# Optimization experiments

Measured on AMD Instinct MI355X. Metric: run time of the kernel, lower is better.

Reference implementation:

```python
import jax, jax.numpy as jnp
import numpy as np

D_MODEL = 1024
NUM_HEADS = 16
SCALE = (D_MODEL // NUM_HEADS) ** -0.5


def setup_inputs() -> dict:
    key = jax.random.key(0)
    ks = jax.random.split(key, 9)
    B, S, D = 4, 2048, D_MODEL
    s = 1.0 / np.sqrt(D)
    x = jax.random.normal(ks[0], (B, S, D), dtype=jnp.float32)
    Wq = jax.random.uniform(ks[1], (D, D), jnp.float32, -s, s)
    bq = jax.random.uniform(ks[2], (D,), jnp.float32, -s, s)
    Wk = jax.random.uniform(ks[3], (D, D), jnp.float32, -s, s)
    bk = jax.random.uniform(ks[4], (D,), jnp.float32, -s, s)
    Wv = jax.random.uniform(ks[5], (D, D), jnp.float32, -s, s)
    bv = jax.random.uniform(ks[6], (D,), jnp.float32, -s, s)
    Wo = jax.random.uniform(ks[7], (D, D), jnp.float32, -s, s)
    bo = jax.random.uniform(ks[8], (D,), jnp.float32, -s, s)
    return {"x": x, "Wq": Wq, "bq": bq, "Wk": Wk, "bk": bk,
            "Wv": Wv, "bv": bv, "Wo": Wo, "bo": bo}


def reference(x, Wq, bq, Wk, bk, Wv, bv, Wo, bo):
    # Linear: x @ W.T + b (torch nn.Linear convention)
    Q = jnp.einsum('bsd,ed->bse', x, Wq) + bq
    K = jnp.einsum('bsd,ed->bse', x, Wk) + bk
    V = jnp.einsum('bsd,ed->bse', x, Wv) + bv
    # Single-head full attention over d_model (module does NOT split heads)
    scores = jnp.einsum('bqd,bkd->bqk', Q, K) * SCALE  # [B,S,S]
    attn = jax.nn.softmax(scores, axis=-1)  # dropout is identity at inference
    out = jnp.einsum('bqk,bkd->bqd', attn, V)
    return jnp.einsum('bsd,ed->bse', out, Wo) + bo
```

## Files before the change

kernel.cpp:

```cpp
#include <hip/hip_runtime.h>
#include <hip/hip_bf16.h>


#define TILE 128
#define BK 32
#define BUFE (TILE * BK)

typedef __attribute__((ext_vector_type(8))) short bf16x8;
typedef __attribute__((ext_vector_type(4))) float f32x4;

__device__ __forceinline__ void stage_tiles(
    const __hip_bfloat16* __restrict__ Ab, const __hip_bfloat16* __restrict__ Bb,
    __hip_bfloat16* As, __hip_bfloat16* Bs,
    long rowBase, long colBase, int K, int k0, int tid)
{
  #pragma unroll
  for (int p = 0; p < 2; ++p) {
    int seg = tid + p * 256;
    int r   = seg >> 2;
    int cq  = seg & 3;
    const __hip_bfloat16* ga = Ab + (rowBase + r) * (long)K + k0 + cq * 8;
    __builtin_amdgcn_global_load_lds(
        (const __attribute__((address_space(1))) void*)ga,
        (__attribute__((address_space(3))) void*)(As + seg * 8), 16, 0, 0);
    const __hip_bfloat16* gb = Bb + (colBase + r) * (long)K + k0 + cq * 8;
    __builtin_amdgcn_global_load_lds(
        (const __attribute__((address_space(1))) void*)gb,
        (__attribute__((address_space(3))) void*)(Bs + seg * 8), 16, 0, 0);
  }
}

__device__ __forceinline__ void gemm_core(
    const __hip_bfloat16* __restrict__ Ab, const __hip_bfloat16* __restrict__ Bb,
    __hip_bfloat16* As, __hip_bfloat16* Bs,
    long rowBase, long colBase, int K, int tid, int wr, int wc, int lr, int q,
    f32x4 acc[4][4])
{
  stage_tiles(Ab, Bb, As, Bs, rowBase, colBase, K, 0, tid);
  int buf = 0;
  for (int k0 = 0; k0 < K; k0 += BK, buf ^= 1) {
    __syncthreads();
    if (k0 + BK < K)
      stage_tiles(Ab, Bb, As + (buf ^ 1) * BUFE, Bs + (buf ^ 1) * BUFE,
                  rowBase, colBase, K, k0 + BK, tid);
    const __hip_bfloat16* Ac = As + buf * BUFE;
    const __hip_bfloat16* Bc = Bs + buf * BUFE;
    bf16x8 af[4], bfr[4];
    #pragma unroll
    for (int mi = 0; mi < 4; ++mi)
      af[mi] = *(const bf16x8*)(Ac + (wr + mi * 16 + lr) * BK + q * 8);
    #pragma unroll
    for (int ni = 0; ni < 4; ++ni)
      bfr[ni] = *(const bf16x8*)(Bc + (wc + ni * 16 + lr) * BK + q * 8);
    #pragma unroll
    for (int mi = 0; mi < 4; ++mi)
      #pragma unroll
      for (int ni = 0; ni < 4; ++ni)
        acc[mi][ni] = __builtin_amdgcn_mfma_f32_16x16x32_bf16(
            af[mi], bfr[ni], acc[mi][ni], 0, 0, 0);
  }
}

__global__ __launch_bounds__(256) void gemm_bt(
    const __hip_bfloat16* __restrict__ A,
    const __hip_bfloat16* __restrict__ B,
    void* __restrict__ Cv,
    const float* __restrict__ bias,
    int K, int ldC,
    long sA, long sB, long sC,
    float scale, int mode)
{
  const long z = blockIdx.z;
  __shared__ __hip_bfloat16 As[2 * BUFE];
  __shared__ __hip_bfloat16 Bs[2 * BUFE];
  const int tid  = threadIdx.x;
  const int lane = tid & 63;
  const int wid  = tid >> 6;
  const int wr   = (wid >> 1) * 64;
  const int wc   = (wid & 1) * 64;
  const int lr   = lane & 15;
  const int q    = lane >> 4;
  const long rowBase = (long)blockIdx.x * TILE;
  const long colBase = (long)blockIdx.y * TILE;

  f32x4 acc[4][4] = {};
  gemm_core(A + z * sA, B + z * sB, As, Bs, rowBase, colBase, K,
            tid, wr, wc, lr, q, acc);

  #pragma unroll
  for (int ni = 0; ni < 4; ++ni) {
    long col = colBase + wc + ni * 16 + lr;
    float bv = bias ? bias[col] : 0.0f;
    #pragma unroll
    for (int mi = 0; mi < 4; ++mi) {
      #pragma unroll
      for (int i = 0; i < 4; ++i) {
        long row = rowBase + wr + mi * 16 + q * 4 + i;
        float v = acc[mi][ni][i] * scale + bv;
        if (mode == 0)
          ((__hip_bfloat16*)Cv)[z * sC + row * (long)ldC + col] = __float2bfloat16(v);
        else
          ((float*)Cv)[z * sC + row * (long)ldC + col] = v;
      }
    }
  }
}

__device__ __forceinline__ void stage_half(
    const __hip_bfloat16* __restrict__ g, __hip_bfloat16* lds,
    long rowBase, int ld, int k0, int tid)
{
  #pragma unroll
  for (int j = 0; j < 2; ++j) {
    int idx = tid + j * 512;
    int r   = idx >> 3;
    int cg  = (idx & 7) ^ (r & 7);
    const __hip_bfloat16* src = g + (rowBase + r) * (long)ld + k0 + cg * 8;
    __builtin_amdgcn_global_load_lds(
        (const __attribute__((address_space(1))) void*)src,
        (__attribute__((address_space(3))) void*)(lds + idx * 8), 16, 0, 0);
  }
}

__device__ __forceinline__ bf16x8 frag256(const __hip_bfloat16* half_, int row, int off)
{
  const char* p = (const char*)half_ + row * 128 + (off ^ ((row & 7) << 4));
  return *(const bf16x8*)p;
}

#define WAITV(N) asm volatile("s_waitcnt vmcnt(" #N ")" ::: "memory")
#define BAR __builtin_amdgcn_s_barrier()

__device__ __forceinline__ void xcd_decode(int NX, int NY, int NZ,
                                           int& bx, int& by, long& z)
{
  const int nwg = NX * NY * NZ;
  int lin = (int)blockIdx.x + NX * ((int)blockIdx.y + NY * (int)blockIdx.z);
  int xcd = lin & 7, off = lin >> 3;
  int q8 = nwg >> 3, r8 = nwg & 7;
  lin = ((xcd < r8) ? xcd * (q8 + 1) : r8 * (q8 + 1) + (xcd - r8) * q8) + off;
  by = lin % NY;
  bx = (lin / NY) % NX;
  z  = lin / (NY * NX);
}

#define READ_A8(BUF, HALF)                                                  \
  _Pragma("unroll")                                                         \
  for (int ks = 0; ks < 2; ++ks)                                            \
    _Pragma("unroll")                                                       \
    for (int mi = 0; mi < 4; ++mi)                                          \
      a[ks * 4 + mi] =                                                      \
          frag256(&L[BUF][0][HALF][0], wr + mi * 16 + lr, ks * 64 + q16);

#define READ_B4(BREG, BUF, HALF)                                            \
  _Pragma("unroll")                                                         \
  for (int ks = 0; ks < 2; ++ks)                                            \
    _Pragma("unroll")                                                       \
    for (int ni = 0; ni < 2; ++ni)                                          \
      BREG[ks * 2 + ni] =                                                   \
          frag256(&L[BUF][1][HALF][0], wc + ni * 16 + lr, ks * 64 + q16);

#define MMA_QUAD(MOFF, NOFF, BREG)                                          \
  __builtin_amdgcn_s_setprio(1);                                            \
  _Pragma("unroll")                                                         \
  for (int ks = 0; ks < 2; ++ks)                                            \
    _Pragma("unroll")                                                       \
    for (int mi = 0; mi < 4; ++mi)                                          \
      _Pragma("unroll")                                                     \
      for (int ni = 0; ni < 2; ++ni)                                        \
        acc[(MOFF) + mi][(NOFF) + ni] =                                     \
            __builtin_amdgcn_mfma_f32_16x16x32_bf16(                        \
                a[ks * 4 + mi], BREG[ks * 2 + ni],                          \
                acc[(MOFF) + mi][(NOFF) + ni], 0, 0, 0);                    \
  __builtin_amdgcn_s_setprio(0);

__global__ __launch_bounds__(512, 2) void gemm256_bt(
    const __hip_bfloat16* __restrict__ A,
    const __hip_bfloat16* __restrict__ B,
    void* __restrict__ Cv,
    const float* __restrict__ bias,
    int K, int ldA, int ldB, int ldC,
    long sA_, long sB_, long sC_,
    float scale, int mode)
{
  __shared__ __hip_bfloat16 L[2][2][2][128 * 64];

  const int tid  = threadIdx.x;
  const int lane = tid & 63;
  const int wid  = tid >> 6;
  const int wr   = (wid >> 2) * 64;
  const int wc   = (wid & 3) * 32;
  const int lr   = lane & 15;
  const int q    = lane >> 4;
  const int q16  = q * 16;

  int bx, by; long z;
  xcd_decode(gridDim.x, gridDim.y, gridDim.z, bx, by, z);

  const long rowBase = (long)bx * 256;
  const long colBase = (long)by * 256;
  const __hip_bfloat16* Ab = A + z * sA_;
  const __hip_bfloat16* Bb = B + z * sB_;

  f32x4 acc[8][4] = {};
  bf16x8 a[8], bA[4], bB[4];
  const int KT = K >> 6;

  {
    const int kk1 = (KT > 1 ? 1 : 0) * 64;
    stage_half(Ab, &L[0][0][0][0], rowBase,       ldA, 0,   tid);
    stage_half(Bb, &L[0][1][0][0], colBase,       ldB, 0,   tid);
    stage_half(Bb, &L[0][1][1][0], colBase + 128, ldB, 0,   tid);
    stage_half(Ab, &L[0][0][1][0], rowBase + 128, ldA, 0,   tid);
    stage_half(Ab, &L[1][0][0][0], rowBase,       ldA, kk1, tid);
    stage_half(Bb, &L[1][1][0][0], colBase,       ldB, kk1, tid);
    WAITV(8);
    BAR;
  }

  for (int kt = 0; kt < KT; ++kt) {
    const int cur = kt & 1, nxt = cur ^ 1;
    const int t1 = kt + 1 < KT ? kt + 1 : KT - 1;
    const int t2 = kt + 2 < KT ? kt + 2 : KT - 1;
    const int k1 = t1 << 6, k2 = t2 << 6;

    stage_half(Bb, &L[nxt][1][1][0], colBase + 128, ldB, k1, tid);
    WAITV(8);
    READ_A8(cur, 0);
    READ_B4(bA, cur, 0);
    BAR;
    MMA_QUAD(0, 0, bA);
    stage_half(Ab, &L[nxt][0][1][0], rowBase + 128, ldA, k1, tid);
    WAITV(8);
    READ_B4(bB, cur, 1);
    BAR;
    MMA_QUAD(0, 2, bB);
    stage_half(Ab, &L[cur][0][0][0], rowBase, ldA, k2, tid);
    WAITV(8);
    READ_A8(cur, 1);
    BAR;
    MMA_QUAD(4, 2, bB);
    stage_half(Bb, &L[cur][1][0][0], colBase, ldB, k2, tid);
    WAITV(8);
    BAR;
    MMA_QUAD(4, 0, bA);
  }
  WAITV(0);

  const long cz = z * sC_;
  #pragma unroll
  for (int n = 0; n < 4; ++n) {
    long col = colBase + (n >> 1) * 128 + wc + (n & 1) * 16 + lr;
    float bv = bias ? bias[col] : 0.0f;
    #pragma unroll
    for (int m = 0; m < 8; ++m) {
      long row0 = rowBase + (m >> 2) * 128 + wr + (m & 3) * 16 + q * 4;
      f32x4 v = acc[m][n];
      #pragma unroll
      for (int i = 0; i < 4; ++i) {
        float val = v[i] * scale + bv;
        if (mode == 0)
          ((__hip_bfloat16*)Cv)[cz + (row0 + i) * (long)ldC + col] =
              __float2bfloat16(val);
        else
          ((float*)Cv)[cz + (row0 + i) * (long)ldC + col] = val;
      }
    }
  }
}

__global__ __launch_bounds__(512, 2) void gemm128_bt(
    const __hip_bfloat16* __restrict__ A,
    const __hip_bfloat16* __restrict__ B,
    void* __restrict__ Cv,
    const float* __restrict__ bias,
    int K, int ldA, int ldB, int ldC,
    long sA_, long sB_, long sC_,
    float scale, int mode)
{
  __shared__ __hip_bfloat16 L[3][3][128 * 64];

  const int tid  = threadIdx.x;
  const int lane = tid & 63;
  const int wid  = tid >> 6;
  const int wr   = (wid >> 2) * 64;
  const int wc   = (wid & 3) * 32;
  const int lr   = lane & 15;
  const int q    = lane >> 4;
  const int q16  = q * 16;

  int bx, by; long z;
  xcd_decode(gridDim.x, gridDim.y, gridDim.z, bx, by, z);

  const long rowBase = (long)bx * 128;
  const long colBase = (long)by * 256;
  const __hip_bfloat16* Ab = A + z * sA_;
  const __hip_bfloat16* Bb = B + z * sB_;

  f32x4 acc[4][4] = {};
  bf16x8 a[8], bA[4], bB[4];
  const int KT = K >> 6;

  {
    const int kk1 = (KT > 1 ? 1 : 0) * 64;
    stage_half(Ab, &L[0][0][0], rowBase,       ldA, 0,   tid);
    stage_half(Bb, &L[0][1][0], colBase,       ldB, 0,   tid);
    stage_half(Bb, &L[0][2][0], colBase + 128, ldB, 0,   tid);
    stage_half(Ab, &L[1][0][0], rowBase,       ldA, kk1, tid);
    stage_half(Bb, &L[1][1][0], colBase,       ldB, kk1, tid);
    stage_half(Bb, &L[1][2][0], colBase + 128, ldB, kk1, tid);
    WAITV(8);
    BAR;
  }

  int cur = 0, nx2 = 2;
  for (int t = 0; t < KT; ++t) {
    const int kc = ((t + 2 < KT) ? (t + 2) : (KT - 1)) << 6;
    stage_half(Ab, &L[nx2][0][0], rowBase,       ldA, kc, tid);
    stage_half(Bb, &L[nx2][1][0], colBase,       ldB, kc, tid);
    WAITV(10);
    #pragma unroll
    for (int ks = 0; ks < 2; ++ks)
      #pragma unroll
      for (int mi = 0; mi < 4; ++mi)
        a[ks * 4 + mi] = frag256(&L[cur][0][0], wr + mi * 16 + lr, ks * 64 + q16);
    #pragma unroll
    for (int ks = 0; ks < 2; ++ks)
      #pragma unroll
      for (int ni = 0; ni < 2; ++ni)
        bA[ks * 2 + ni] = frag256(&L[cur][1][0], wc + ni * 16 + lr, ks * 64 + q16);
    BAR;
    __builtin_amdgcn_s_setprio(1);
    #pragma unroll
    for (int ks = 0; ks < 2; ++ks)
      #pragma unroll
      for (int mi = 0; mi < 4; ++mi)
        #pragma unroll
        for (int ni = 0; ni < 2; ++ni)
          acc[mi][ni] = __builtin_amdgcn_mfma_f32_16x16x32_bf16(
              a[ks * 4 + mi], bA[ks * 2 + ni], acc[mi][ni], 0, 0, 0);
    __builtin_amdgcn_s_setprio(0);
    stage_half(Bb, &L[nx2][2][0], colBase + 128, ldB, kc, tid);
    WAITV(8);
    #pragma unroll
    for (int ks = 0; ks < 2; ++ks)
      #pragma unroll
      for (int ni = 0; ni < 2; ++ni)
        bB[ks * 2 + ni] = frag256(&L[cur][2][0], wc + ni * 16 + lr, ks * 64 + q16);
    BAR;
    __builtin_amdgcn_s_setprio(1);
    #pragma unroll
    for (int ks = 0; ks < 2; ++ks)
      #pragma unroll
      for (int mi = 0; mi < 4; ++mi)
        #pragma unroll
        for (int ni = 0; ni < 2; ++ni)
          acc[mi][2 + ni] = __builtin_amdgcn_mfma_f32_16x16x32_bf16(
              a[ks * 4 + mi], bB[ks * 2 + ni], acc[mi][2 + ni], 0, 0, 0);
    __builtin_amdgcn_s_setprio(0);
    cur = (cur == 2) ? 0 : cur + 1;
    nx2 = (nx2 == 2) ? 0 : nx2 + 1;
  }
  WAITV(0);

  const long cz = z * sC_;
  #pragma unroll
  for (int n = 0; n < 4; ++n) {
    long col = colBase + (n >> 1) * 128 + wc + (n & 1) * 16 + lr;
    float bv = bias ? bias[col] : 0.0f;
    #pragma unroll
    for (int m = 0; m < 4; ++m) {
      long row0 = rowBase + wr + m * 16 + q * 4;
      f32x4 v = acc[m][n];
      #pragma unroll
      for (int i = 0; i < 4; ++i) {
        float val = v[i] * scale + bv;
        if (mode == 0)
          ((__hip_bfloat16*)Cv)[cz + (row0 + i) * (long)ldC + col] =
              __float2bfloat16(val);
        else
          ((float*)Cv)[cz + (row0 + i) * (long)ldC + col] = val;
      }
    }
  }
}

__global__ __launch_bounds__(256) void cvt_f32_bf16(
    const float* __restrict__ in, __hip_bfloat16* __restrict__ out)
{
  long i = ((long)blockIdx.x * 256 + threadIdx.x) * 8;
  float4 a = *(const float4*)(in + i);
  float4 b = *(const float4*)(in + i + 4);
  bf16x8 o;
  o[0] = __builtin_bit_cast(short, __float2bfloat16(a.x));
  o[1] = __builtin_bit_cast(short, __float2bfloat16(a.y));
  o[2] = __builtin_bit_cast(short, __float2bfloat16(a.z));
  o[3] = __builtin_bit_cast(short, __float2bfloat16(a.w));
  o[4] = __builtin_bit_cast(short, __float2bfloat16(b.x));
  o[5] = __builtin_bit_cast(short, __float2bfloat16(b.y));
  o[6] = __builtin_bit_cast(short, __float2bfloat16(b.z));
  o[7] = __builtin_bit_cast(short, __float2bfloat16(b.w));
  *(bf16x8*)(out + i) = o;
}

__global__ __launch_bounds__(256) void cvt_t_f32_bf16(
    const float* __restrict__ in, __hip_bfloat16* __restrict__ out)
{
  __shared__ __hip_bfloat16 t[64][65];
  const int tid = threadIdx.x;
  const long rb = (long)blockIdx.y * 64;
  const long cb = (long)blockIdx.x * 64;
  const int r0 = tid >> 4;
  const int c0 = (tid & 15) * 4;
  #pragma unroll
  for (int p = 0; p < 4; ++p) {
    int r = r0 + p * 16;
    float4 v = *(const float4*)(in + (rb + r) * 1024 + cb + c0);
    t[c0 + 0][r] = __float2bfloat16(v.x);
    t[c0 + 1][r] = __float2bfloat16(v.y);
    t[c0 + 2][r] = __float2bfloat16(v.z);
    t[c0 + 3][r] = __float2bfloat16(v.w);
  }
  __syncthreads();
  #pragma unroll
  for (int p = 0; p < 4; ++p) {
    int r = r0 + p * 16;
    __hip_bfloat16* o = out + (cb + r) * 1024 + rb + c0;
    o[0] = t[r][c0 + 0]; o[1] = t[r][c0 + 1];
    o[2] = t[r][c0 + 2]; o[3] = t[r][c0 + 3];
  }
}

__global__ __launch_bounds__(256) void bias_vo(
    const float* __restrict__ Wo, const float* __restrict__ bv,
    const float* __restrict__ bo, float* __restrict__ bfinal)
{
  int e = blockIdx.x * 4 + (threadIdx.x >> 6);
  int lane = threadIdx.x & 63;
  const float* row = Wo + (long)e * 1024;
  float s = 0.0f;
  #pragma unroll
  for (int p = 0; p < 4; ++p) {
    float4 w = *(const float4*)(row + p * 256 + lane * 4);
    float4 b = *(const float4*)(bv + p * 256 + lane * 4);
    s += w.x * b.x + w.y * b.y + w.z * b.z + w.w * b.w;
  }
  #pragma unroll
  for (int o = 32; o; o >>= 1) s += __shfl_xor(s, o);
  if (lane == 0) bfinal[e] = s + bo[e];
}

__global__ __launch_bounds__(256) void cat_bias(
    const float* __restrict__ a, const float* __restrict__ b,
    float* __restrict__ o)
{
  int i = blockIdx.x * 256 + threadIdx.x;
  o[i] = (i < 1024) ? a[i] : b[i - 1024];
}

__global__ __launch_bounds__(256) void softmax_rows(__hip_bfloat16* __restrict__ P)
{
  const int tid  = threadIdx.x;
  const int lane = tid & 63;
  const int wid  = tid >> 6;
  __hip_bfloat16* p = P + (long)blockIdx.x * 2048 + tid * 8;

  bf16x8 v = *(const bf16x8*)p;
  float x[8];
  #pragma unroll
  for (int i = 0; i < 8; ++i)
    x[i] = __uint_as_float(((unsigned)(unsigned short)v[i]) << 16);

  float m = x[0];
  #pragma unroll
  for (int i = 1; i < 8; ++i) m = fmaxf(m, x[i]);
  #pragma unroll
  for (int o = 32; o; o >>= 1) m = fmaxf(m, __shfl_xor(m, o));

  __shared__ float rmax[4], rsum[4];
  if (lane == 0) rmax[wid] = m;
  __syncthreads();
  m = fmaxf(fmaxf(rmax[0], rmax[1]), fmaxf(rmax[2], rmax[3]));

  float e[8], s = 0.0f;
  #pragma unroll
  for (int i = 0; i < 8; ++i) { e[i] = __expf(x[i] - m); s += e[i]; }
  #pragma unroll
  for (int o = 32; o; o >>= 1) s += __shfl_xor(s, o);
  if (lane == 0) rsum[wid] = s;
  __syncthreads();
  s = (rsum[0] + rsum[1]) + (rsum[2] + rsum[3]);

  float inv = 1.0f / s;
  bf16x8 ov;
  #pragma unroll
  for (int i = 0; i < 8; ++i) {
    __hip_bfloat16 h = __float2bfloat16(e[i] * inv);
    ov[i] = __builtin_bit_cast(short, h);
  }
  *(bf16x8*)p = ov;
}

extern "C" void kernel_launch(void* const* d_in, const int* in_sizes, int n_in,
                              void* d_out, int out_size, void* d_ws, size_t ws_size,
                              hipStream_t stream) {
  const float* x  = (const float*)d_in[0];
  const float* Wq = (const float*)d_in[1];
  const float* bq = (const float*)d_in[2];
  const float* Wk = (const float*)d_in[3];
  const float* bk = (const float*)d_in[4];
  const float* Wv = (const float*)d_in[5];
  const float* bv = (const float*)d_in[6];
  const float* Wo = (const float*)d_in[7];
  const float* bo = (const float*)d_in[8];
  float* out = (float*)d_out;

  const long B = 4, S = 2048, D = 1024;
  char* ws = (char*)d_ws;
  __hip_bfloat16* xb   = (__hip_bfloat16*)ws; ws += B * S * D * 2;
  __hip_bfloat16* Wqkb = (__hip_bfloat16*)ws; ws += 2 * D * D * 2;
  __hip_bfloat16* Wob  = (__hip_bfloat16*)ws; ws += D * D * 2;
  __hip_bfloat16* QK   = (__hip_bfloat16*)ws; ws += (B * S) * (2 * D) * 2;
  __hip_bfloat16* VWot = (__hip_bfloat16*)ws; ws += B * D * S * 2;
  __hip_bfloat16* P    = (__hip_bfloat16*)ws; ws += B * S * S * 2;
  __hip_bfloat16* Wvtb   = QK;
  __hip_bfloat16* Wvo    = P;
  float*          bfinal = (float*)Wob;
  float*          bqk    = (float*)Wob + 1024;

  dim3 blk(256);
  dim3 blk5(512);
  cvt_f32_bf16<<<dim3(4096), blk, 0, stream>>>(x,  xb);
  cvt_f32_bf16<<<dim3(512),  blk, 0, stream>>>(Wq, Wqkb);
  cvt_f32_bf16<<<dim3(512),  blk, 0, stream>>>(Wk, Wqkb + D * D);
  cvt_f32_bf16<<<dim3(512),  blk, 0, stream>>>(Wo, Wob);
  cvt_t_f32_bf16<<<dim3(16, 16), blk, 0, stream>>>(Wv, Wvtb);

  gemm_bt<<<dim3(8, 8, 1), blk, 0, stream>>>(Wob, Wvtb, Wvo,
                                             nullptr, 1024, 1024, 0, 0, 0, 1.0f, 0);
  bias_vo<<<dim3(256), blk, 0, stream>>>(Wo, bv, bo, bfinal);
  cat_bias<<<dim3(8), blk, 0, stream>>>(bq, bk, bqk);

  gemm256_bt<<<dim3(32, 8, 1), blk5, 0, stream>>>(
      xb, Wqkb, QK, bqk, 1024, 1024, 1024, 2048, 0, 0, 0, 1.0f, 0);
  gemm128_bt<<<dim3(8, 8, 4), blk5, 0, stream>>>(
      Wvo, xb, VWot, nullptr, 1024, 1024, 1024, 2048, 0, S * D, D * S, 1.0f, 0);
  gemm256_bt<<<dim3(8, 8, 4), blk5, 0, stream>>>(
      QK, QK + 1024, P, nullptr, 1024, 2048, 2048, 2048,
      S * 2048, S * 2048, S * S, 0.125f, 0);
  softmax_rows<<<dim3(8192), blk, 0, stream>>>(P);
  gemm128_bt<<<dim3(16, 4, 4), blk5, 0, stream>>>(
      P, VWot, out, bfinal, 2048, 2048, 2048, 1024,
      S * S, D * S, S * D, 1.0f, 2);
}
```

Baseline: 278.6 us.

## Run 256-tile GEMM with 1024 threads and fuse small prep kernels

```diff
diff --git a/kernel.cpp b/kernel.cpp
--- a/kernel.cpp
+++ b/kernel.cpp
@@ -122,6 +122,18 @@
   }
 }
 
+__device__ __forceinline__ void stage_half_1k(
+    const __hip_bfloat16* __restrict__ g, __hip_bfloat16* lds,
+    long rowBase, int ld, int k0, int tid)
+{
+  int r  = tid >> 3;
+  int cg = (tid & 7) ^ (r & 7);
+  const __hip_bfloat16* src = g + (rowBase + r) * (long)ld + k0 + cg * 8;
+  __builtin_amdgcn_global_load_lds(
+      (const __attribute__((address_space(1))) void*)src,
+      (__attribute__((address_space(3))) void*)(lds + tid * 8), 16, 0, 0);
+}
+
 __device__ __forceinline__ bf16x8 frag256(const __hip_bfloat16* half_, int row, int off)
 {
   const char* p = (const char*)half_ + row * 128 + (off ^ ((row & 7) << 4));
@@ -144,37 +156,7 @@
   z  = lin / (NY * NX);
 }
 
-#define READ_A8(BUF, HALF)                                                  \
-  _Pragma("unroll")                                                         \
-  for (int ks = 0; ks < 2; ++ks)                                            \
-    _Pragma("unroll")                                                       \
-    for (int mi = 0; mi < 4; ++mi)                                          \
-      a[ks * 4 + mi] =                                                      \
-          frag256(&L[BUF][0][HALF][0], wr + mi * 16 + lr, ks * 64 + q16);
-
-#define READ_B4(BREG, BUF, HALF)                                            \
-  _Pragma("unroll")                                                         \
-  for (int ks = 0; ks < 2; ++ks)                                            \
-    _Pragma("unroll")                                                       \
-    for (int ni = 0; ni < 2; ++ni)                                          \
-      BREG[ks * 2 + ni] =                                                   \
-          frag256(&L[BUF][1][HALF][0], wc + ni * 16 + lr, ks * 64 + q16);
-
-#define MMA_QUAD(MOFF, NOFF, BREG)                                          \
-  __builtin_amdgcn_s_setprio(1);                                            \
-  _Pragma("unroll")                                                         \
-  for (int ks = 0; ks < 2; ++ks)                                            \
-    _Pragma("unroll")                                                       \
-    for (int mi = 0; mi < 4; ++mi)                                          \
-      _Pragma("unroll")                                                     \
-      for (int ni = 0; ni < 2; ++ni)                                        \
-        acc[(MOFF) + mi][(NOFF) + ni] =                                     \
-            __builtin_amdgcn_mfma_f32_16x16x32_bf16(                        \
-                a[ks * 4 + mi], BREG[ks * 2 + ni],                          \
-                acc[(MOFF) + mi][(NOFF) + ni], 0, 0, 0);                    \
-  __builtin_amdgcn_s_setprio(0);
-
-__global__ __launch_bounds__(512, 2) void gemm256_bt(
+__global__ __launch_bounds__(1024, 1) void gemm256_bt(
     const __hip_bfloat16* __restrict__ A,
     const __hip_bfloat16* __restrict__ B,
     void* __restrict__ Cv,
@@ -188,8 +170,8 @@
   const int tid  = threadIdx.x;
   const int lane = tid & 63;
   const int wid  = tid >> 6;
-  const int wr   = (wid >> 2) * 64;
-  const int wc   = (wid & 3) * 32;
+  const int wrr  = (wid >> 2) * 32;
+  const int wcc  = (wid & 3) * 32;
   const int lr   = lane & 15;
   const int q    = lane >> 4;
   const int q16  = q * 16;
@@ -202,19 +184,19 @@
   const __hip_bfloat16* Ab = A + z * sA_;
   const __hip_bfloat16* Bb = B + z * sB_;
 
-  f32x4 acc[8][4] = {};
-  bf16x8 a[8], bA[4], bB[4];
+  f32x4 acc[4][4] = {};
+  bf16x8 a[4], bA[4], bB[4];
   const int KT = K >> 6;
 
   {
     const int kk1 = (KT > 1 ? 1 : 0) * 64;
-    stage_half(Ab, &L[0][0][0][0], rowBase,       ldA, 0,   tid);
-    stage_half(Bb, &L[0][1][0][0], colBase,       ldB, 0,   tid);
-    stage_half(Bb, &L[0][1][1][0], colBase + 128, ldB, 0,   tid);
-    stage_half(Ab, &L[0][0][1][0], rowBase + 128, ldA, 0,   tid);
-    stage_half(Ab, &L[1][0][0][0], rowBase,       ldA, kk1, tid);
-    stage_half(Bb, &L[1][1][0][0], colBase,       ldB, kk1, tid);
-    WAITV(8);
+    stage_half_1k(Ab, &L[0][0][0][0], rowBase,       ldA, 0,   tid);
+    stage_half_1k(Bb, &L[0][1][0][0], colBase,       ldB, 0,   tid);
+    stage_half_1k(Bb, &L[0][1][1][0], colBase + 128, ldB, 0,   tid);
+    stage_half_1k(Ab, &L[0][0][1][0], rowBase + 128, ldA, 0,   tid);
+    stage_half_1k(Ab, &L[1][0][0][0], rowBase,       ldA, kk1, tid);
+    stage_half_1k(Bb, &L[1][1][0][0], colBase,       ldB, kk1, tid);
+    WAITV(4);
     BAR;
   }
 
@@ -224,37 +206,93 @@
     const int t2 = kt + 2 < KT ? kt + 2 : KT - 1;
     const int k1 = t1 << 6, k2 = t2 << 6;
 
-    stage_half(Bb, &L[nxt][1][1][0], colBase + 128, ldB, k1, tid);
-    WAITV(8);
-    READ_A8(cur, 0);
-    READ_B4(bA, cur, 0);
-    BAR;
-    MMA_QUAD(0, 0, bA);
-    stage_half(Ab, &L[nxt][0][1][0], rowBase + 128, ldA, k1, tid);
-    WAITV(8);
-    READ_B4(bB, cur, 1);
-    BAR;
-    MMA_QUAD(0, 2, bB);
-    stage_half(Ab, &L[cur][0][0][0], rowBase, ldA, k2, tid);
-    WAITV(8);
-    READ_A8(cur, 1);
-    BAR;
-    MMA_QUAD(4, 2, bB);
-    stage_half(Bb, &L[cur][1][0][0], colBase, ldB, k2, tid);
-    WAITV(8);
-    BAR;
-    MMA_QUAD(4, 0, bA);
+    stage_half_1k(Bb, &L[nxt][1][1][0], colBase + 128, ldB, k1, tid);
+    WAITV(4);
+    #pragma unroll
+    for (int ks = 0; ks < 2; ++ks)
+      #pragma unroll
+      for (int mi = 0; mi < 2; ++mi)
+        a[ks * 2 + mi] =
+            frag256(&L[cur][0][0][0], wrr + mi * 16 + lr, ks * 64 + q16);
+    #pragma unroll
+    for (int ks = 0; ks < 2; ++ks)
+      #pragma unroll
+      for (int ni = 0; ni < 2; ++ni)
+        bA[ks * 2 + ni] =
+            frag256(&L[cur][1][0][0], wcc + ni * 16 + lr, ks * 64 + q16);
+    BAR;
+    __builtin_amdgcn_s_setprio(1);
+    #pragma unroll
+    for (int ks = 0; ks < 2; ++ks)
+      #pragma unroll
+      for (int mi = 0; mi < 2; ++mi)
+        #pragma unroll
+        for (int ni = 0; ni < 2; ++ni)
+          acc[mi][ni] = __builtin_amdgcn_mfma_f32_16x16x32_bf16(
+              a[ks * 2 + mi], bA[ks * 2 + ni], acc[mi][ni], 0, 0, 0);
+    __builtin_amdgcn_s_setprio(0);
+    stage_half_1k(Ab, &L[nxt][0][1][0], rowBase + 128, ldA, k1, tid);
+    WAITV(4);
+    #pragma unroll
+    for (int ks = 0; ks < 2; ++ks)
+      #pragma unroll
+      for (int ni = 0; ni < 2; ++ni)
+        bB[ks * 2 + ni] =
+            frag256(&L[cur][1][1][0], wcc + ni * 16 + lr, ks * 64 + q16);
+    BAR;
+    __builtin_amdgcn_s_setprio(1);
+    #pragma unroll
+    for (int ks = 0; ks < 2; ++ks)
+      #pragma unroll
+      for (int mi = 0; mi < 2; ++mi)
+        #pragma unroll
+        for (int ni = 0; ni < 2; ++ni)
+          acc[mi][2 + ni] = __builtin_amdgcn_mfma_f32_16x16x32_bf16(
+              a[ks * 2 + mi], bB[ks * 2 + ni], acc[mi][2 + ni], 0, 0, 0);
+    __builtin_amdgcn_s_setprio(0);
+    stage_half_1k(Ab, &L[cur][0][0][0], rowBase, ldA, k2, tid);
+    WAITV(4);
+    #pragma unroll
+    for (int ks = 0; ks < 2; ++ks)
+      #pragma unroll
+      for (int mi = 0; mi < 2; ++mi)
+        a[ks * 2 + mi] =
+            frag256(&L[cur][0][1][0], wrr + mi * 16 + lr, ks * 64 + q16);
+    BAR;
+    __builtin_amdgcn_s_setprio(1);
+    #pragma unroll
+    for (int ks = 0; ks < 2; ++ks)
+      #pragma unroll
+      for (int mi = 0; mi < 2; ++mi)
+        #pragma unroll
+        for (int ni = 0; ni < 2; ++ni)
+          acc[2 + mi][2 + ni] = __builtin_amdgcn_mfma_f32_16x16x32_bf16(
+              a[ks * 2 + mi], bB[ks * 2 + ni], acc[2 + mi][2 + ni], 0, 0, 0);
+    __builtin_amdgcn_s_setprio(0);
+    stage_half_1k(Bb, &L[cur][1][0][0], colBase, ldB, k2, tid);
+    WAITV(4);
+    BAR;
+    __builtin_amdgcn_s_setprio(1);
+    #pragma unroll
+    for (int ks = 0; ks < 2; ++ks)
+      #pragma unroll
+      for (int mi = 0; mi < 2; ++mi)
+        #pragma unroll
+        for (int ni = 0; ni < 2; ++ni)
+          acc[2 + mi][ni] = __builtin_amdgcn_mfma_f32_16x16x32_bf16(
+              a[ks * 2 + mi], bA[ks * 2 + ni], acc[2 + mi][ni], 0, 0, 0);
+    __builtin_amdgcn_s_setprio(0);
   }
   WAITV(0);
 
   const long cz = z * sC_;
   #pragma unroll
   for (int n = 0; n < 4; ++n) {
-    long col = colBase + (n >> 1) * 128 + wc + (n & 1) * 16 + lr;
+    long col = colBase + (n >> 1) * 128 + wcc + (n & 1) * 16 + lr;
     float bv = bias ? bias[col] : 0.0f;
     #pragma unroll
-    for (int m = 0; m < 8; ++m) {
-      long row0 = rowBase + (m >> 2) * 128 + wr + (m & 3) * 16 + q * 4;
+    for (int m = 0; m < 4; ++m) {
+      long row0 = rowBase + (m >> 1) * 128 + wrr + (m & 1) * 16 + q * 4;
       f32x4 v = acc[m][n];
       #pragma unroll
       for (int i = 0; i < 4; ++i) {
@@ -403,6 +441,32 @@
   *(bf16x8*)(out + i) = o;
 }
 
+__global__ __launch_bounds__(256) void cvt_w3_f32_bf16(
+    const float* __restrict__ Wq, const float* __restrict__ Wk,
+    const float* __restrict__ Wo,
+    __hip_bfloat16* __restrict__ oQ, __hip_bfloat16* __restrict__ oK,
+    __hip_bfloat16* __restrict__ oO)
+{
+  int blk = blockIdx.x;
+  const float* in; __hip_bfloat16* out;
+  if (blk < 512)        { in = Wq; out = oQ; }
+  else if (blk < 1024)  { in = Wk; out = oK; blk -= 512; }
+  else                  { in = Wo; out = oO; blk -= 1024; }
+  long i = ((long)blk * 256 + threadIdx.x) * 8;
+  float4 a = *(const float4*)(in + i);
+  float4 b = *(const float4*)(in + i + 4);
+  bf16x8 o;
+  o[0] = __builtin_bit_cast(short, __float2bfloat16(a.x));
+  o[1] = __builtin_bit_cast(short, __float2bfloat16(a.y));
+  o[2] = __builtin_bit_cast(short, __float2bfloat16(a.z));
+  o[3] = __builtin_bit_cast(short, __float2bfloat16(a.w));
+  o[4] = __builtin_bit_cast(short, __float2bfloat16(b.x));
+  o[5] = __builtin_bit_cast(short, __float2bfloat16(b.y));
+  o[6] = __builtin_bit_cast(short, __float2bfloat16(b.z));
+  o[7] = __builtin_bit_cast(short, __float2bfloat16(b.w));
+  *(bf16x8*)(out + i) = o;
+}
+
 __global__ __launch_bounds__(256) void cvt_t_f32_bf16(
     const float* __restrict__ in, __hip_bfloat16* __restrict__ out)
 {
@@ -431,31 +495,31 @@
   }
 }
 
-__global__ __launch_bounds__(256) void bias_vo(
+__global__ __launch_bounds__(256) void bias_fuse(
     const float* __restrict__ Wo, const float* __restrict__ bv,
-    const float* __restrict__ bo, float* __restrict__ bfinal)
-{
-  int e = blockIdx.x * 4 + (threadIdx.x >> 6);
-  int lane = threadIdx.x & 63;
-  const float* row = Wo + (long)e * 1024;
-  float s = 0.0f;
-  #pragma unroll
-  for (int p = 0; p < 4; ++p) {
-    float4 w = *(const float4*)(row + p * 256 + lane * 4);
-    float4 b = *(const float4*)(bv + p * 256 + lane * 4);
-    s += w.x * b.x + w.y * b.y + w.z * b.z + w.w * b.w;
-  }
-  #pragma unroll
-  for (int o = 32; o; o >>= 1) s += __shfl_xor(s, o);
-  if (lane == 0) bfinal[e] = s + bo[e];
-}
-
-__global__ __launch_bounds__(256) void cat_bias(
-    const float* __restrict__ a, const float* __restrict__ b,
-    float* __restrict__ o)
-{
-  int i = blockIdx.x * 256 + threadIdx.x;
-  o[i] = (i < 1024) ? a[i] : b[i - 1024];
+    const float* __restrict__ bo, const float* __restrict__ bq,
+    const float* __restrict__ bk, float* __restrict__ bfinal,
+    float* __restrict__ bqk)
+{
+  int blk = blockIdx.x;
+  if (blk < 256) {
+    int e = blk * 4 + (threadIdx.x >> 6);
+    int lane = threadIdx.x & 63;
+    const float* row = Wo + (long)e * 1024;
+    float s = 0.0f;
+    #pragma unroll
+    for (int p = 0; p < 4; ++p) {
+      float4 w = *(const float4*)(row + p * 256 + lane * 4);
+      float4 b = *(const float4*)(bv + p * 256 + lane * 4);
+      s += w.x * b.x + w.y * b.y + w.z * b.z + w.w * b.w;
+    }
+    #pragma unroll
+    for (int o = 32; o; o >>= 1) s += __shfl_xor(s, o);
+    if (lane == 0) bfinal[e] = s + bo[e];
+  } else {
+    int i = (blk - 256) * 256 + threadIdx.x;
+    bqk[i] = (i < 1024) ? bq[i] : bk[i - 1024];
+  }
 }
 
 __global__ __launch_bounds__(256) void softmax_rows(__hip_bfloat16* __restrict__ P)
@@ -530,22 +594,21 @@
 
   dim3 blk(256);
   dim3 blk5(512);
-  cvt_f32_bf16<<<dim3(4096), blk, 0, stream>>>(x,  xb);
-  cvt_f32_bf16<<<dim3(512),  blk, 0, stream>>>(Wq, Wqkb);
-  cvt_f32_bf16<<<dim3(512),  blk, 0, stream>>>(Wk, Wqkb + D * D);
-  cvt_f32_bf16<<<dim3(512),  blk, 0, stream>>>(Wo, Wob);
+  dim3 blkX(1024);
+  cvt_f32_bf16<<<dim3(4096), blk, 0, stream>>>(x, xb);
+  cvt_w3_f32_bf16<<<dim3(1536), blk, 0, stream>>>(Wq, Wk, Wo,
+                                                  Wqkb, Wqkb + D * D, Wob);
   cvt_t_f32_bf16<<<dim3(16, 16), blk, 0, stream>>>(Wv, Wvtb);
 
   gemm_bt<<<dim3(8, 8, 1), blk, 0, stream>>>(Wob, Wvtb, Wvo,
                                              nullptr, 1024, 1024, 0, 0, 0, 1.0f, 0);
-  bias_vo<<<dim3(256), blk, 0, stream>>>(Wo, bv, bo, bfinal);
-  cat_bias<<<dim3(8), blk, 0, stream>>>(bq, bk, bqk);
-
-  gemm256_bt<<<dim3(32, 8, 1), blk5, 0, stream>>>(
+  bias_fuse<<<dim3(264), blk, 0, stream>>>(Wo, bv, bo, bq, bk, bfinal, bqk);
+
+  gemm256_bt<<<dim3(32, 8, 1), blkX, 0, stream>>>(
       xb, Wqkb, QK, bqk, 1024, 1024, 1024, 2048, 0, 0, 0, 1.0f, 0);
   gemm128_bt<<<dim3(8, 8, 4), blk5, 0, stream>>>(
       Wvo, xb, VWot, nullptr, 1024, 1024, 1024, 2048, 0, S * D, D * S, 1.0f, 0);
-  gemm256_bt<<<dim3(8, 8, 4), blk5, 0, stream>>>(
+  gemm256_bt<<<dim3(8, 8, 4), blkX, 0, stream>>>(
       QK, QK + 1024, P, nullptr, 1024, 2048, 2048, 2048,
       S * 2048, S * 2048, S * S, 0.125f, 0);
   softmax_rows<<<dim3(8192), blk, 0, stream>>>(P);
```

Measured after the change: 288.5 us. 3.6% more time.

## Split-K the Wo·Wv product, merge weight conversions and bias kernels

Applied to the files above, without the earlier changes.

```diff
diff --git a/kernel.cpp b/kernel.cpp
--- a/kernel.cpp
+++ b/kernel.cpp
@@ -2,109 +2,9 @@
 #include <hip/hip_bf16.h>
 
 
-#define TILE 128
-#define BK 32
-#define BUFE (TILE * BK)
-
 typedef __attribute__((ext_vector_type(8))) short bf16x8;
+typedef __attribute__((ext_vector_type(4))) short bf16x4;
 typedef __attribute__((ext_vector_type(4))) float f32x4;
-
-__device__ __forceinline__ void stage_tiles(
-    const __hip_bfloat16* __restrict__ Ab, const __hip_bfloat16* __restrict__ Bb,
-    __hip_bfloat16* As, __hip_bfloat16* Bs,
-    long rowBase, long colBase, int K, int k0, int tid)
-{
-  #pragma unroll
-  for (int p = 0; p < 2; ++p) {
-    int seg = tid + p * 256;
-    int r   = seg >> 2;
-    int cq  = seg & 3;
-    const __hip_bfloat16* ga = Ab + (rowBase + r) * (long)K + k0 + cq * 8;
-    __builtin_amdgcn_global_load_lds(
-        (const __attribute__((address_space(1))) void*)ga,
-        (__attribute__((address_space(3))) void*)(As + seg * 8), 16, 0, 0);
-    const __hip_bfloat16* gb = Bb + (colBase + r) * (long)K + k0 + cq * 8;
-    __builtin_amdgcn_global_load_lds(
-        (const __attribute__((address_space(1))) void*)gb,
-        (__attribute__((address_space(3))) void*)(Bs + seg * 8), 16, 0, 0);
-  }
-}
-
-__device__ __forceinline__ void gemm_core(
-    const __hip_bfloat16* __restrict__ Ab, const __hip_bfloat16* __restrict__ Bb,
-    __hip_bfloat16* As, __hip_bfloat16* Bs,
-    long rowBase, long colBase, int K, int tid, int wr, int wc, int lr, int q,
-    f32x4 acc[4][4])
-{
-  stage_tiles(Ab, Bb, As, Bs, rowBase, colBase, K, 0, tid);
-  int buf = 0;
-  for (int k0 = 0; k0 < K; k0 += BK, buf ^= 1) {
-    __syncthreads();
-    if (k0 + BK < K)
-      stage_tiles(Ab, Bb, As + (buf ^ 1) * BUFE, Bs + (buf ^ 1) * BUFE,
-                  rowBase, colBase, K, k0 + BK, tid);
-    const __hip_bfloat16* Ac = As + buf * BUFE;
-    const __hip_bfloat16* Bc = Bs + buf * BUFE;
-    bf16x8 af[4], bfr[4];
-    #pragma unroll
-    for (int mi = 0; mi < 4; ++mi)
-      af[mi] = *(const bf16x8*)(Ac + (wr + mi * 16 + lr) * BK + q * 8);
-    #pragma unroll
-    for (int ni = 0; ni < 4; ++ni)
-      bfr[ni] = *(const bf16x8*)(Bc + (wc + ni * 16 + lr) * BK + q * 8);
-    #pragma unroll
-    for (int mi = 0; mi < 4; ++mi)
-      #pragma unroll
-      for (int ni = 0; ni < 4; ++ni)
-        acc[mi][ni] = __builtin_amdgcn_mfma_f32_16x16x32_bf16(
-            af[mi], bfr[ni], acc[mi][ni], 0, 0, 0);
-  }
-}
-
-__global__ __launch_bounds__(256) void gemm_bt(
-    const __hip_bfloat16* __restrict__ A,
-    const __hip_bfloat16* __restrict__ B,
-    void* __restrict__ Cv,
-    const float* __restrict__ bias,
-    int K, int ldC,
-    long sA, long sB, long sC,
-    float scale, int mode)
-{
-  const long z = blockIdx.z;
-  __shared__ __hip_bfloat16 As[2 * BUFE];
-  __shared__ __hip_bfloat16 Bs[2 * BUFE];
-  const int tid  = threadIdx.x;
-  const int lane = tid & 63;
-  const int wid  = tid >> 6;
-  const int wr   = (wid >> 1) * 64;
-  const int wc   = (wid & 1) * 64;
-  const int lr   = lane & 15;
-  const int q    = lane >> 4;
-  const long rowBase = (long)blockIdx.x * TILE;
-  const long colBase = (long)blockIdx.y * TILE;
-
-  f32x4 acc[4][4] = {};
-  gemm_core(A + z * sA, B + z * sB, As, Bs, rowBase, colBase, K,
-            tid, wr, wc, lr, q, acc);
-
-  #pragma unroll
-  for (int ni = 0; ni < 4; ++ni) {
-    long col = colBase + wc + ni * 16 + lr;
-    float bv = bias ? bias[col] : 0.0f;
-    #pragma unroll
-    for (int mi = 0; mi < 4; ++mi) {
-      #pragma unroll
-      for (int i = 0; i < 4; ++i) {
-        long row = rowBase + wr + mi * 16 + q * 4 + i;
-        float v = acc[mi][ni][i] * scale + bv;
-        if (mode == 0)
-          ((__hip_bfloat16*)Cv)[z * sC + row * (long)ldC + col] = __float2bfloat16(v);
-        else
-          ((float*)Cv)[z * sC + row * (long)ldC + col] = v;
-      }
-    }
-  }
-}
 
 __device__ __forceinline__ void stage_half(
     const __hip_bfloat16* __restrict__ g, __hip_bfloat16* lds,
@@ -403,6 +303,32 @@
   *(bf16x8*)(out + i) = o;
 }
 
+__global__ __launch_bounds__(256) void cvt_w3_f32_bf16(
+    const float* __restrict__ Wq, const float* __restrict__ Wk,
+    const float* __restrict__ Wo,
+    __hip_bfloat16* __restrict__ oQ, __hip_bfloat16* __restrict__ oK,
+    __hip_bfloat16* __restrict__ oO)
+{
+  int blk = blockIdx.x;
+  const float* in; __hip_bfloat16* out;
+  if (blk < 512)        { in = Wq; out = oQ; }
+  else if (blk < 1024)  { in = Wk; out = oK; blk -= 512; }
+  else                  { in = Wo; out = oO; blk -= 1024; }
+  long i = ((long)blk * 256 + threadIdx.x) * 8;
+  float4 a = *(const float4*)(in + i);
+  float4 b = *(const float4*)(in + i + 4);
+  bf16x8 o;
+  o[0] = __builtin_bit_cast(short, __float2bfloat16(a.x));
+  o[1] = __builtin_bit_cast(short, __float2bfloat16(a.y));
+  o[2] = __builtin_bit_cast(short, __float2bfloat16(a.z));
+  o[3] = __builtin_bit_cast(short, __float2bfloat16(a.w));
+  o[4] = __builtin_bit_cast(short, __float2bfloat16(b.x));
+  o[5] = __builtin_bit_cast(short, __float2bfloat16(b.y));
+  o[6] = __builtin_bit_cast(short, __float2bfloat16(b.z));
+  o[7] = __builtin_bit_cast(short, __float2bfloat16(b.w));
+  *(bf16x8*)(out + i) = o;
+}
+
 __global__ __launch_bounds__(256) void cvt_t_f32_bf16(
     const float* __restrict__ in, __hip_bfloat16* __restrict__ out)
 {
@@ -431,31 +357,48 @@
   }
 }
 
-__global__ __launch_bounds__(256) void bias_vo(
+__global__ __launch_bounds__(256) void reduce_wvo(
+    const float* __restrict__ p, __hip_bfloat16* __restrict__ out)
+{
+  const long S1 = 1024L * 1024L;
+  long i = ((long)blockIdx.x * 256 + threadIdx.x) * 4;
+  float4 a = *(const float4*)(p + i);
+  float4 b = *(const float4*)(p + i + S1);
+  float4 c = *(const float4*)(p + i + 2 * S1);
+  float4 d = *(const float4*)(p + i + 3 * S1);
+  bf16x4 o;
+  o[0] = __builtin_bit_cast(short, __float2bfloat16(a.x + b.x + c.x + d.x));
+  o[1] = __builtin_bit_cast(short, __float2bfloat16(a.y + b.y + c.y + d.y));
+  o[2] = __builtin_bit_cast(short, __float2bfloat16(a.z + b.z + c.z + d.z));
+  o[3] = __builtin_bit_cast(short, __float2bfloat16(a.w + b.w + c.w + d.w));
+  *(bf16x4*)(out + i) = o;
+}
+
+__global__ __launch_bounds__(256) void bias_fuse(
     const float* __restrict__ Wo, const float* __restrict__ bv,
-    const float* __restrict__ bo, float* __restrict__ bfinal)
-{
-  int e = blockIdx.x * 4 + (threadIdx.x >> 6);
-  int lane = threadIdx.x & 63;
-  const float* row = Wo + (long)e * 1024;
-  float s = 0.0f;
-  #pragma unroll
-  for (int p = 0; p < 4; ++p) {
-    float4 w = *(const float4*)(row + p * 256 + lane * 4);
-    float4 b = *(const float4*)(bv + p * 256 + lane * 4);
-    s += w.x * b.x + w.y * b.y + w.z * b.z + w.w * b.w;
-  }
-  #pragma unroll
-  for (int o = 32; o; o >>= 1) s += __shfl_xor(s, o);
-  if (lane == 0) bfinal[e] = s + bo[e];
-}
-
-__global__ __launch_bounds__(256) void cat_bias(
-    const float* __restrict__ a, const float* __restrict__ b,
-    float* __restrict__ o)
-{
-  int i = blockIdx.x * 256 + threadIdx.x;
-  o[i] = (i < 1024) ? a[i] : b[i - 1024];
+    const float* __restrict__ bo, const float* __restrict__ bq,
+    const float* __restrict__ bk, float* __restrict__ bfinal,
+    float* __restrict__ bqk)
+{
+  int blk = blockIdx.x;
+  if (blk < 256) {
+    int e = blk * 4 + (threadIdx.x >> 6);
+    int lane = threadIdx.x & 63;
+    const float* row = Wo + (long)e * 1024;
+    float s = 0.0f;
+    #pragma unroll
+    for (int p = 0; p < 4; ++p) {
+      float4 w = *(const float4*)(row + p * 256 + lane * 4);
+      float4 b = *(const float4*)(bv + p * 256 + lane * 4);
+      s += w.x * b.x + w.y * b.y + w.z * b.z + w.w * b.w;
+    }
+    #pragma unroll
+    for (int o = 32; o; o >>= 1) s += __shfl_xor(s, o);
+    if (lane == 0) bfinal[e] = s + bo[e];
+  } else {
+    int i = (blk - 256) * 256 + threadIdx.x;
+    bqk[i] = (i < 1024) ? bq[i] : bk[i - 1024];
+  }
 }
 
 __global__ __launch_bounds__(256) void softmax_rows(__hip_bfloat16* __restrict__ P)
@@ -524,22 +467,23 @@
   __hip_bfloat16* VWot = (__hip_bfloat16*)ws; ws += B * D * S * 2;
   __hip_bfloat16* P    = (__hip_bfloat16*)ws; ws += B * S * S * 2;
   __hip_bfloat16* Wvtb   = QK;
+  float*          Wvop   = (float*)(QK + 2 * D * D);
   __hip_bfloat16* Wvo    = P;
   float*          bfinal = (float*)Wob;
   float*          bqk    = (float*)Wob + 1024;
 
   dim3 blk(256);
   dim3 blk5(512);
-  cvt_f32_bf16<<<dim3(4096), blk, 0, stream>>>(x,  xb);
-  cvt_f32_bf16<<<dim3(512),  blk, 0, stream>>>(Wq, Wqkb);
-  cvt_f32_bf16<<<dim3(512),  blk, 0, stream>>>(Wk, Wqkb + D * D);
-  cvt_f32_bf16<<<dim3(512),  blk, 0, stream>>>(Wo, Wob);
+  cvt_f32_bf16<<<dim3(4096), blk, 0, stream>>>(x, xb);
+  cvt_w3_f32_bf16<<<dim3(1536), blk, 0, stream>>>(Wq, Wk, Wo,
+                                                  Wqkb, Wqkb + D * D, Wob);
   cvt_t_f32_bf16<<<dim3(16, 16), blk, 0, stream>>>(Wv, Wvtb);
 
-  gemm_bt<<<dim3(8, 8, 1), blk, 0, stream>>>(Wob, Wvtb, Wvo,
-                                             nullptr, 1024, 1024, 0, 0, 0, 1.0f, 0);
-  bias_vo<<<dim3(256), blk, 0, stream>>>(Wo, bv, bo, bfinal);
-  cat_bias<<<dim3(8), blk, 0, stream>>>(bq, bk, bqk);
+  gemm128_bt<<<dim3(8, 4, 4), blk5, 0, stream>>>(
+      Wob, Wvtb, Wvop, nullptr, 256, 1024, 1024, 1024,
+      256, 256, 1024L * 1024L, 1.0f, 2);
+  reduce_wvo<<<dim3(1024), blk, 0, stream>>>(Wvop, Wvo);
+  bias_fuse<<<dim3(264), blk, 0, stream>>>(Wo, bv, bo, bq, bk, bfinal, bqk);
 
   gemm256_bt<<<dim3(32, 8, 1), blk5, 0, stream>>>(
       xb, Wqkb, QK, bqk, 1024, 1024, 1024, 2048, 0, 0, 0, 1.0f, 0);
```

Measured after the change: 260.2 us. 1.07x faster.
